# Performance work log

Measured on AMD Instinct MI355X. Metric: run time of the kernel, lower is better.

Reference implementation:

```python
import jax, jax.numpy as jnp
import numpy as np

B, N, INC, H, W = 1, 6, 256, 56, 100
DD, CC = 41, 64                         # depth bins (4..45 step 1), cam feat channels
NX, NY, NZ = 33, 33, 2                  # BEV grid from pc_range=[-50,-50,-5,50,50,3], grid=3
CZ = CC * NZ                            # 128 channels into bevencode
DXV = jnp.array([3.0, 3.0, 3.0], jnp.float32)
BXV = jnp.array([-48.5, -48.5, -3.5], jnp.float32)


def _frustum():
    ds = jnp.arange(4.0, 45.0, 1.0)                      # (41,)
    xs = jnp.linspace(0.0, 1599.0, W)
    ys = jnp.linspace(0.0, 899.0, H)
    d = jnp.broadcast_to(ds[:, None, None], (DD, H, W))
    xg = jnp.broadcast_to(xs[None, None, :], (DD, H, W))
    yg = jnp.broadcast_to(ys[None, :, None], (DD, H, W))
    return jnp.stack([xg, yg, d], -1)                    # (D,H,W,3)


def _conv(x, w):
    return jax.lax.conv_general_dilated(x, w, (1, 1), 'SAME',
                                        dimension_numbers=('NCHW', 'OIHW', 'NCHW'))


def _bn_relu(x, s, b, m, v):
    inv = s / jnp.sqrt(v + 1e-5)
    return jax.nn.relu(x * inv[None, :, None, None] + (b - m * inv)[None, :, None, None])


def _forward(x, rots, trans, dn_w, dn_b,
             bw1, bn1_s, bn1_b, bn1_m, bn1_v,
             bw2, bn2_s, bn2_b, bn2_m, bn2_v,
             bw3, bn3_s, bn3_b, bn3_m, bn3_v,
             bw4, bn4_s, bn4_b, bn4_m, bn4_v):
    # ---- CamEncode: 1x1 depthnet -> softmax depth dist + context features ----
    xf = x.reshape(B * N, INC, H, W)
    y = _conv(xf, dn_w) + dn_b[None, :, None, None]
    depth = jax.nn.softmax(y[:, :DD], axis=1).reshape(B, N, DD, H, W)
    feat = y[:, DD:DD + CC].reshape(B, N, CC, H, W)
    # ---- get_geometry: (u*d, v*d, d) -> ego frame ----
    fr = _frustum()                                                     # (D,H,W,3)
    pts = jnp.concatenate([fr[..., :2] * fr[..., 2:3], fr[..., 2:3]], -1)
    geom = jnp.einsum('bnij,dhwj->bndhwi', rots, pts) + trans[:, :, None, None, None, :]
    # ---- voxel indices (torch .long() truncates toward zero) ----
    coor = ((geom - (BXV - DXV / 2.0)) / DXV).astype(jnp.int32)         # (B,N,D,H,W,3)
    cx, cy, cz = coor[..., 0], coor[..., 1], coor[..., 2]
    kept = (cx >= 0) & (cx < NX) & (cy >= 0) & (cy < NY) & (cz >= 0) & (cz < NZ)
    bidx = jnp.arange(B, dtype=jnp.int32)[:, None, None, None, None]
    ranks = ((bidx * NZ + cz) * NY + cy) * NX + cx                      # bev rank per point
    nvox = B * NZ * NY * NX
    seg = jnp.where(kept, ranks, nvox).reshape(-1)                      # drop bucket = nvox
    # ---- lift: depth-weighted outer product, splat: segment-sum by voxel ----
    vol = depth[..., None] * feat.transpose(0, 1, 3, 4, 2)[:, :, None]  # (B,N,D,H,W,C)
    bev = jax.ops.segment_sum(vol.reshape(-1, CC), seg, num_segments=nvox + 1)[:nvox]
    bev = bev.reshape(B, NZ, NY, NX, CC).transpose(0, 4, 1, 2, 3).reshape(B, CZ, NY, NX)
    h = _bn_relu(_conv(bev, bw1), bn1_s, bn1_b, bn1_m, bn1_v)
    h = _bn_relu(_conv(h, bw2), bn2_s, bn2_b, bn2_m, bn2_v)
    h = _bn_relu(_conv(h, bw3), bn3_s, bn3_b, bn3_m, bn3_v)
    h = _bn_relu(_conv(h, bw4), bn4_s, bn4_b, bn4_m, bn4_v)
    return h                                                            # (B,256,33,33)


def setup_inputs() -> dict:
    key = jax.random.key(0)
    ks = jax.random.split(key, 16)
    x = jax.random.normal(ks[0], (B, N, INC, H, W), jnp.float32)
    # rots = small rotation perturbation composed with intrinsics inverse
    kinv = jnp.array([[1.0 / 800.0, 0.0, -1.0], [0.0, 1.0 / 800.0, -0.5625], [0.0, 0.0, 1.0]], jnp.float32)
    R = jnp.eye(3, dtype=jnp.float32) + 0.05 * jax.random.normal(ks[1], (B, N, 3, 3), jnp.float32)
    rots = jnp.einsum('bnij,jk->bnik', R, kinv)
    trans = 2.0 * jax.random.normal(ks[2], (B, N, 3), jnp.float32)

    def w(k, o, i, kh, kw):
        return jax.random.normal(k, (o, i, kh, kw), jnp.float32) * (2.0 / (i * kh * kw)) ** 0.5

    def bn(k, c):
        k1, k2, k3, k4 = jax.random.split(k, 4)
        return (1.0 + 0.1 * jax.random.normal(k1, (c,), jnp.float32),
                0.1 * jax.random.normal(k2, (c,), jnp.float32),
                0.1 * jax.random.normal(k3, (c,), jnp.float32),
                jax.random.uniform(k4, (c,), jnp.float32, 0.5, 1.5))
    bn1 = bn(ks[7], CZ); bn2 = bn(ks[8], 512); bn3 = bn(ks[9], 512); bn4 = bn(ks[10], 256)
    return dict(
        x=x, rots=rots, trans=trans,
        dn_w=w(ks[3], DD + CC, INC, 1, 1), dn_b=jnp.zeros((DD + CC,), jnp.float32),
        bw1=w(ks[4], CZ, CZ, 3, 3),
        bn1_s=bn1[0], bn1_b=bn1[1], bn1_m=bn1[2], bn1_v=bn1[3],
        bw2=w(ks[5], 512, CZ, 3, 3),
        bn2_s=bn2[0], bn2_b=bn2[1], bn2_m=bn2[2], bn2_v=bn2[3],
        bw3=w(ks[6], 512, 512, 3, 3),
        bn3_s=bn3[0], bn3_b=bn3[1], bn3_m=bn3[2], bn3_v=bn3[3],
        bw4=w(ks[11], 256, 512, 3, 3),
        bn4_s=bn4[0], bn4_b=bn4[1], bn4_m=bn4[2], bn4_v=bn4[3])


def reference(x, rots, trans, dn_w, dn_b,
              bw1, bn1_s, bn1_b, bn1_m, bn1_v,
              bw2, bn2_s, bn2_b, bn2_m, bn2_v,
              bw3, bn3_s, bn3_b, bn3_m, bn3_v,
              bw4, bn4_s, bn4_b, bn4_m, bn4_v):
    return _forward(x, rots, trans, dn_w, dn_b,
                    bw1, bn1_s, bn1_b, bn1_m, bn1_v,
                    bw2, bn2_s, bn2_b, bn2_m, bn2_v,
                    bw3, bn3_s, bn3_b, bn3_m, bn3_v,
                    bw4, bn4_s, bn4_b, bn4_m, bn4_v)
```

## Files before the change

kernel.cpp:

```cpp
#include <hip/hip_runtime.h>
#include <math.h>

#define NCAM  6
#define INC   256
#define HH    56
#define WW    100
#define HW    5600
#define NPIX  33600
#define DDEP  41
#define CFEAT 64
#define NCH   105
#define NXG   33
#define NYG   33
#define NZG   2
#define NVOX  2178
#define PADW  35
#define PADHW 1225
#define NPIXO 1089

typedef short bf16x8 __attribute__((ext_vector_type(8)));
typedef float f32x4  __attribute__((ext_vector_type(4)));

#define Y_OFF    0
#define Y_SZ     (NCAM * NCH * HW)
#define WDH_OFF  (Y_OFF + Y_SZ)
#define WDL_OFF  (WDH_OFF + 16384)
#define W1H_OFF  (WDL_OFF + 16384)
#define W1L_OFF  (W1H_OFF + 73728)
#define W2H_OFF  (W1L_OFF + 73728)
#define W2L_OFF  (W2H_OFF + 294912)
#define W3H_OFF  (W2L_OFF + 294912)
#define W3L_OFF  (W3H_OFF + 1179648)
#define W4H_OFF  (W3L_OFF + 1179648)
#define W4L_OFF  (W4H_OFF + 589824)
#define BEV_OFF  (W4L_OFF + 589824)
#define BEV_SZ   (NVOX * CFEAT)
#define A0_OFF   (BEV_OFF + BEV_SZ)
#define A1_OFF   (A0_OFF + 78400)
#define A2_OFF   (A1_OFF + 78400)
#define A3_OFF   (A2_OFF + 313600)
#define P_OFF    (A3_OFF + 313600)
#define P_SZ     4460544
#define WS_END   (P_OFF + P_SZ)

__device__ __forceinline__ unsigned short f2bf_rn(float f) {
    unsigned u = __builtin_bit_cast(unsigned, f);
    unsigned r = (u + 0x7FFFu + ((u >> 16) & 1u)) >> 16;
    return (unsigned short)r;
}
__device__ __forceinline__ void split_bf(float f, unsigned short& h, unsigned short& l) {
    h = f2bf_rn(f);
    float hf = __builtin_bit_cast(float, (unsigned)h << 16);
    l = f2bf_rn(f - hf);
}
__device__ __forceinline__ void split_bf_trunc(float f, short& h, short& l) {
    unsigned u = __builtin_bit_cast(unsigned, f);
    h = (short)(u >> 16);
    float hf = __builtin_bit_cast(float, u & 0xFFFF0000u);
    float r = f - hf;
    l = (short)(__builtin_bit_cast(unsigned, r) >> 16);
}

__device__ __forceinline__ void wprep_conv(const float* __restrict__ wgt,
                                           unsigned short* __restrict__ wh,
                                           unsigned short* __restrict__ wl,
                                           int COUT, int CIN, int i)
{
    int jj = i & 7, lane = (i >> 3) & 63;
    int r  = i >> 9;
    int nchk = CIN >> 5;
    int chk = r % nchk; r /= nchk;
    int ncog = COUT >> 4;
    int cog = r % ncog; int dydx = r / ncog;
    int co = cog * 16 + (lane & 15);
    int ci = chk * 32 + (lane >> 4) * 8 + jj;
    float w = wgt[((size_t)co * CIN + ci) * 9 + dydx];
    unsigned short h, l; split_bf(w, h, l);
    wh[i] = h; wl[i] = l;
}

__global__ __launch_bounds__(256) void k_wprep_all(const float* __restrict__ dnw,
                                                   const float* __restrict__ bw1,
                                                   const float* __restrict__ bw2,
                                                   const float* __restrict__ bw3,
                                                   const float* __restrict__ bw4,
                                                   unsigned short* __restrict__ wdh,
                                                   unsigned short* __restrict__ wdl,
                                                   unsigned short* __restrict__ w1h,
                                                   unsigned short* __restrict__ w1l,
                                                   unsigned short* __restrict__ w2h,
                                                   unsigned short* __restrict__ w2l,
                                                   unsigned short* __restrict__ w3h,
                                                   unsigned short* __restrict__ w3l,
                                                   unsigned short* __restrict__ w4h,
                                                   unsigned short* __restrict__ w4l)
{
    int i = blockIdx.x * 256 + threadIdx.x;
    if (i < 32768) {
        int jj = i & 7, lane = (i >> 3) & 63, chk = (i >> 9) & 7, ct = i >> 12;
        int co = ct * 16 + (lane & 15);
        int ci = chk * 32 + (lane >> 4) * 8 + jj;
        float w = (co < NCH) ? dnw[co * 256 + ci] : 0.f;
        unsigned short h, l; split_bf(w, h, l);
        wdh[i] = h; wdl[i] = l;
        return;
    }
    i -= 32768;
    if (i < 147456)  { wprep_conv(bw1, w1h, w1l, 128, 128, i); return; }
    i -= 147456;
    if (i < 589824)  { wprep_conv(bw2, w2h, w2l, 512, 128, i); return; }
    i -= 589824;
    if (i < 2359296) { wprep_conv(bw3, w3h, w3l, 512, 512, i); return; }
    i -= 2359296;
    if (i < 1179648) { wprep_conv(bw4, w4h, w4l, 256, 512, i); return; }
}

__global__ __launch_bounds__(256) void k_depthnet_fused(const float* __restrict__ x,
                                                        const unsigned short* __restrict__ wdh,
                                                        const unsigned short* __restrict__ wdl,
                                                        const float* __restrict__ dnb,
                                                        float* __restrict__ y)
{
    const int t  = threadIdx.x;
    const int w  = t >> 6;
    const int l  = t & 63;
    const int lp = l & 15;
    const int q  = l >> 4;
    const int n   = blockIdx.y;
    const int ct0 = blockIdx.z * 4;
    const int px  = blockIdx.x * 64 + w * 16 + lp;
    const bool pok = px < HW;
    const float* xl = x + (size_t)n * INC * HW + (pok ? px : 0);

    f32x4 acc[4];
#pragma unroll
    for (int ct = 0; ct < 4; ++ct) acc[ct] = (f32x4){0.f, 0.f, 0.f, 0.f};

#pragma unroll 2
    for (int ci0 = 0; ci0 < INC; ci0 += 32) {
        float bv[8];
#pragma unroll
        for (int jj = 0; jj < 8; ++jj)
            bv[jj] = xl[(size_t)(ci0 + q * 8 + jj) * HW];
        bf16x8 Bh, Bl;
#pragma unroll
        for (int jj = 0; jj < 8; ++jj) {
            short h, lo; split_bf_trunc(pok ? bv[jj] : 0.f, h, lo);
            Bh[jj] = h; Bl[jj] = lo;
        }
#pragma unroll
        for (int ct = 0; ct < 4; ++ct) {
            const size_t ab = (size_t)(((ct0 + ct) * 8 + (ci0 >> 5)) * 64 + l) * 8;
            bf16x8 Ah = *(const bf16x8*)&wdh[ab];
            bf16x8 Al = *(const bf16x8*)&wdl[ab];
            acc[ct] = __builtin_amdgcn_mfma_f32_16x16x32_bf16(Ah, Bh, acc[ct], 0, 0, 0);
            acc[ct] = __builtin_amdgcn_mfma_f32_16x16x32_bf16(Ah, Bl, acc[ct], 0, 0, 0);
            acc[ct] = __builtin_amdgcn_mfma_f32_16x16x32_bf16(Al, Bh, acc[ct], 0, 0, 0);
        }
    }

    float v[4][4];
#pragma unroll
    for (int ct = 0; ct < 4; ++ct)
#pragma unroll
        for (int j = 0; j < 4; ++j) {
            int co = (ct0 + ct) * 16 + q * 4 + j;
            v[ct][j] = acc[ct][j] + ((co < NCH) ? dnb[co] : 0.f);
        }

    if (ct0 == 0) {
        float m = -3.4e38f;
#pragma unroll
        for (int ct = 0; ct < 4; ++ct)
#pragma unroll
            for (int j = 0; j < 4; ++j) {
                int co = ct * 16 + q * 4 + j;
                if (co < DDEP) m = fmaxf(m, v[ct][j]);
            }
        m = fmaxf(m, __shfl_xor(m, 16));
        m = fmaxf(m, __shfl_xor(m, 32));
        float e[4][4];
        float s = 0.f;
#pragma unroll
        for (int ct = 0; ct < 4; ++ct)
#pragma unroll
            for (int j = 0; j < 4; ++j) {
                int co = ct * 16 + q * 4 + j;
                e[ct][j] = (co < DDEP) ? expf(v[ct][j] - m) : 0.f;
                s += e[ct][j];
            }
        s += __shfl_xor(s, 16);
        s += __shfl_xor(s, 32);
#pragma unroll
        for (int ct = 0; ct < 4; ++ct)
#pragma unroll
            for (int j = 0; j < 4; ++j) {
                int co = ct * 16 + q * 4 + j;
                if (co < DDEP) v[ct][j] = e[ct][j] / s;
            }
    }

    if (pok) {
#pragma unroll
        for (int ct = 0; ct < 4; ++ct)
#pragma unroll
            for (int j = 0; j < 4; ++j) {
                int co = (ct0 + ct) * 16 + q * 4 + j;
                if (co < NCH)
                    y[((size_t)n * NCH + co) * HW + px] = v[ct][j];
            }
    }
}

__global__ __launch_bounds__(256) void k_splat2(const float* __restrict__ y,
                                                const float* __restrict__ rots,
                                                const float* __restrict__ trans,
                                                float* __restrict__ bev)
{
    __shared__ int vox[32 * DDEP];
    const int t  = threadIdx.x;
    const int p0 = blockIdx.x * 32;

    for (int k = t; k < 32 * DDEP; k += 256) {
        int pl = k / DDEP, d = k - pl * DDEP;
        int p = p0 + pl;
        int vx = -1;
        {
            int n = p / HW, hw = p - n * HW;
            int wi = hw % WW, hi = hw / WW;
            const float su = 1599.0f / 99.0f;
            const float sv = 899.0f / 55.0f;
            float u = __fmul_rn((float)wi, su);
            float v = __fmul_rn((float)hi, sv);
            const float* r = rots + n * 9;
            const float* tr = trans + n * 3;
            float dd  = 4.0f + (float)d;
            float pxv = __fmul_rn(u, dd);
            float pyv = __fmul_rn(v, dd);
            float gx = __fadd_rn(__fadd_rn(__fadd_rn(__fmul_rn(r[0], pxv), __fmul_rn(r[1], pyv)), __fmul_rn(r[2], dd)), tr[0]);
            float gy = __fadd_rn(__fadd_rn(__fadd_rn(__fmul_rn(r[3], pxv), __fmul_rn(r[4], pyv)), __fmul_rn(r[5], dd)), tr[1]);
            float gz = __fadd_rn(__fadd_rn(__fadd_rn(__fmul_rn(r[6], pxv), __fmul_rn(r[7], pyv)), __fmul_rn(r[8], dd)), tr[2]);
            int cx = (int)__fdiv_rn(__fadd_rn(gx, 50.0f), 3.0f);
            int cy = (int)__fdiv_rn(__fadd_rn(gy, 50.0f), 3.0f);
            int cz = (int)__fdiv_rn(__fadd_rn(gz, 5.0f), 3.0f);
            if (cx >= 0 && cx < NXG && cy >= 0 && cy < NYG && cz >= 0 && cz < NZG)
                vx = (cz * NYG + cy) * NXG + cx;
        }
        vox[k] = vx;
    }
    __syncthreads();

    const int g  = t >> 5;
    const int pl = t & 31;
    const int p  = p0 + pl;
    int n = p / HW, hw = p - n * HW;
    const float* dbase = y + (size_t)n * NCH * HW + hw;
    const float* fbase = dbase + (size_t)DDEP * HW;
    float f[8];
#pragma unroll
    for (int j = 0; j < 8; ++j) f[j] = fbase[(size_t)(g * 8 + j) * HW];

    float a[8];
#pragma unroll
    for (int j = 0; j < 8; ++j) a[j] = 0.f;
    int cur = -1;
    for (int d = 0; d < DDEP; ++d) {
        int vx = vox[pl * DDEP + d];
        if (vx != cur) {
            if (cur >= 0) {
                float* vp = bev + (size_t)cur * CFEAT + g * 8;
#pragma unroll
                for (int j = 0; j < 8; ++j) atomicAdd(vp + j, a[j]);
            }
            cur = vx;
#pragma unroll
            for (int j = 0; j < 8; ++j) a[j] = 0.f;
        }
        if (vx >= 0) {
            float dval = dbase[(size_t)d * HW];
#pragma unroll
            for (int j = 0; j < 8; ++j) a[j] += __fmul_rn(dval, f[j]);
        }
    }
    if (cur >= 0) {
        float* vp = bev + (size_t)cur * CFEAT + g * 8;
#pragma unroll
        for (int j = 0; j < 8; ++j) atomicAdd(vp + j, a[j]);
    }
}

__global__ __launch_bounds__(256) void k_bev2act(const float* __restrict__ bev,
                                                 unsigned short* __restrict__ a0)
{
    int i = blockIdx.x * 256 + threadIdx.x;
    if (i >= NVOX * CFEAT) return;
    int vx = i >> 6, c = i & 63;
    int cz = vx / NPIXO, rem = vx - cz * NPIXO;
    int yy = rem / NXG, xx = rem - yy * NXG;
    int ch = c * 2 + cz;
    int pos = (yy + 1) * PADW + xx + 1;
    a0[pos * 128 + ch] = f2bf_rn(bev[i]);
}

template<int CIN, int COUT, int SL>
__global__ __launch_bounds__(256) void k_conv_mfma(const unsigned short* __restrict__ act,
                                                   const unsigned short* __restrict__ wh,
                                                   const unsigned short* __restrict__ wl,
                                                   float* __restrict__ P)
{
    constexpr int CI_PER = CIN / SL;
    constexpr int CHUNKS = CI_PER / 32;
    constexpr int NSLOT  = CHUNKS * 4;
    constexpr int SMASK  = NSLOT - 1;
    constexpr int ROW    = NSLOT * 8;
    constexpr int NCOB = COUT / 64;
    constexpr int G    = NCOB * SL;
    constexpr int GX   = G / 8;
    constexpr int POSN = 140;
    __shared__ unsigned short bs[POSN * ROW];
    const int t  = threadIdx.x;
    const int w  = t >> 6;
    const int l  = t & 63;
    const int lp = l & 15;
    const int q  = l >> 4;

    const int bid   = blockIdx.x;
    const int xcd   = bid & 7;
    const int slot  = bid >> 3;
    const int ytile = slot % 17;
    const int gon   = slot / 17;
    const int group = xcd * GX + gon;
    const int cobi  = group % NCOB;
    const int sl    = group / NCOB;

    const int y0  = ytile * 2;
    const int cob = cobi * 64 + w * 16;
    const int ci_base = sl * CI_PER;

    int  pos0[5];
    bool vld[5];
#pragma unroll
    for (int ct = 0; ct < 5; ++ct) {
        int tp = ct * 16 + lp;
        int r = tp / 33, c = tp - r * 33;
        bool v = (tp < 66) && (y0 + r < 33);
        vld[ct]  = v;
        pos0[ct] = v ? (r * 35 + c) : 0;
    }

    for (int i = t; i < POSN * NSLOT; i += 256) {
        int pos = i / NSLOT, s = i - pos * NSLOT;
        int gpos = y0 * 35 + pos;
        int sp = s ^ (pos & SMASK);
        uint4 val = make_uint4(0u, 0u, 0u, 0u);
        if (gpos < PADHW)
            val = *(const uint4*)&act[(size_t)gpos * CIN + ci_base + s * 8];
        *(uint4*)&bs[pos * ROW + sp * 8] = val;
    }
    __syncthreads();

    f32x4 acc[5];
#pragma unroll
    for (int ct = 0; ct < 5; ++ct) acc[ct] = (f32x4){0.f, 0.f, 0.f, 0.f};

#pragma unroll 3
    for (int dydx = 0; dydx < 9; ++dydx) {
        int dy = dydx / 3, dx = dydx - dy * 3;
        int off = dy * 35 + dx;
        bf16x8 Ah[CHUNKS], Al[CHUNKS];
#pragma unroll
        for (int c = 0; c < CHUNKS; ++c) {
            const size_t abase = (size_t)(((dydx * (COUT >> 4) + (cob >> 4)) * (CIN >> 5)
                                           + (ci_base >> 5) + c) * 64 + l) * 8;
            Ah[c] = *(const bf16x8*)&wh[abase];
            Al[c] = *(const bf16x8*)&wl[abase];
        }
#pragma unroll
        for (int ct = 0; ct < 5; ++ct) {
            int pos = pos0[ct] + off;
#pragma unroll
            for (int c = 0; c < CHUNKS; ++c) {
                int sph = (c * 4 + q) ^ (pos & SMASK);
                bf16x8 B = *(const bf16x8*)&bs[pos * ROW + sph * 8];
                acc[ct] = __builtin_amdgcn_mfma_f32_16x16x32_bf16(Ah[c], B, acc[ct], 0, 0, 0);
                acc[ct] = __builtin_amdgcn_mfma_f32_16x16x32_bf16(Al[c], B, acc[ct], 0, 0, 0);
            }
        }
    }

#pragma unroll
    for (int ct = 0; ct < 5; ++ct) {
        if (!vld[ct]) continue;
        int gp = y0 * 33 + ct * 16 + lp;
        float* dst = P + ((size_t)sl * NPIXO + gp) * COUT + cob + q * 4;
        *(f32x4*)dst = acc[ct];
    }
}

template<int SL>
__global__ __launch_bounds__(256) void k_finish(const float* __restrict__ P,
                                                const float* __restrict__ bns,
                                                const float* __restrict__ bnb,
                                                const float* __restrict__ bnm,
                                                const float* __restrict__ bnv,
                                                unsigned short* __restrict__ oact,
                                                float* __restrict__ outf,
                                                int COUT)
{
    int i = blockIdx.x * 256 + threadIdx.x;
    if (i >= COUT * NPIXO) return;
    int co = i % COUT, p = i / COUT;
    float s = 0.f;
#pragma unroll
    for (int sl = 0; sl < SL; ++sl)
        s += P[((size_t)sl * NPIXO + p) * COUT + co];
    float sc = bns[co] / sqrtf(bnv[co] + 1e-5f);
    float bi = bnb[co] - bnm[co] * sc;
    float rv = fmaxf(fmaf(s, sc, bi), 0.f);
    if (outf) {
        outf[(size_t)co * NPIXO + p] = rv;
    } else {
        int yy = p / NXG, xx = p - yy * NXG;
        int pos = (yy + 1) * PADW + xx + 1;
        oact[(size_t)pos * COUT + co] = f2bf_rn(rv);
    }
}

extern "C" void kernel_launch(void* const* d_in, const int* in_sizes, int n_in,
                              void* d_out, int out_size, void* d_ws, size_t ws_size,
                              hipStream_t stream)
{
    const float* x     = (const float*)d_in[0];
    const float* rots  = (const float*)d_in[1];
    const float* trans = (const float*)d_in[2];
    const float* dnw   = (const float*)d_in[3];
    const float* dnb   = (const float*)d_in[4];
    const float* bw1   = (const float*)d_in[5];
    const float* bn1s  = (const float*)d_in[6];
    const float* bn1b  = (const float*)d_in[7];
    const float* bn1m  = (const float*)d_in[8];
    const float* bn1v  = (const float*)d_in[9];
    const float* bw2   = (const float*)d_in[10];
    const float* bn2s  = (const float*)d_in[11];
    const float* bn2b  = (const float*)d_in[12];
    const float* bn2m  = (const float*)d_in[13];
    const float* bn2v  = (const float*)d_in[14];
    const float* bw3   = (const float*)d_in[15];
    const float* bn3s  = (const float*)d_in[16];
    const float* bn3b  = (const float*)d_in[17];
    const float* bn3m  = (const float*)d_in[18];
    const float* bn3v  = (const float*)d_in[19];
    const float* bw4   = (const float*)d_in[20];
    const float* bn4s  = (const float*)d_in[21];
    const float* bn4b  = (const float*)d_in[22];
    const float* bn4m  = (const float*)d_in[23];
    const float* bn4v  = (const float*)d_in[24];

    float* ws  = (float*)d_ws;
    float* y   = ws + Y_OFF;
    float* bev = ws + BEV_OFF;
    float* P   = ws + P_OFF;
    unsigned short* wdh = (unsigned short*)(ws + WDH_OFF);
    unsigned short* wdl = (unsigned short*)(ws + WDL_OFF);
    unsigned short* w1h = (unsigned short*)(ws + W1H_OFF);
    unsigned short* w1l = (unsigned short*)(ws + W1L_OFF);
    unsigned short* w2h = (unsigned short*)(ws + W2H_OFF);
    unsigned short* w2l = (unsigned short*)(ws + W2L_OFF);
    unsigned short* w3h = (unsigned short*)(ws + W3H_OFF);
    unsigned short* w3l = (unsigned short*)(ws + W3L_OFF);
    unsigned short* w4h = (unsigned short*)(ws + W4H_OFF);
    unsigned short* w4l = (unsigned short*)(ws + W4L_OFF);
    unsigned short* a0  = (unsigned short*)(ws + A0_OFF);
    unsigned short* a1  = (unsigned short*)(ws + A1_OFF);
    unsigned short* a2  = (unsigned short*)(ws + A2_OFF);
    unsigned short* a3  = (unsigned short*)(ws + A3_OFF);
    float* out = (float*)d_out;

    hipMemsetAsync(bev, 0, (size_t)(P_OFF - BEV_OFF) * sizeof(float), stream);

    k_wprep_all<<<16832, 256, 0, stream>>>(dnw, bw1, bw2, bw3, bw4,
                                           wdh, wdl, w1h, w1l, w2h, w2l,
                                           w3h, w3l, w4h, w4l);
    k_depthnet_fused<<<dim3(88, 6, 2), 256, 0, stream>>>(x, wdh, wdl, dnb, y);
    k_splat2<<<1050, 256, 0, stream>>>(y, rots, trans, bev);

    k_bev2act<<<(NVOX * CFEAT + 255) / 256, 256, 0, stream>>>(bev, a0);

    k_conv_mfma<128, 128, 4><<<136, 256, 0, stream>>>(a0, w1h, w1l, P);
    k_finish<4><<<(128 * NPIXO + 255) / 256, 256, 0, stream>>>(P, bn1s, bn1b, bn1m, bn1v, a1, nullptr, 128);
    k_conv_mfma<128, 512, 4><<<544, 256, 0, stream>>>(a1, w2h, w2l, P);
    k_finish<4><<<(512 * NPIXO + 255) / 256, 256, 0, stream>>>(P, bn2s, bn2b, bn2m, bn2v, a2, nullptr, 512);
    k_conv_mfma<512, 512, 8><<<1088, 256, 0, stream>>>(a2, w3h, w3l, P);
    k_finish<8><<<(512 * NPIXO + 255) / 256, 256, 0, stream>>>(P, bn3s, bn3b, bn3m, bn3v, a3, nullptr, 512);
    k_conv_mfma<512, 256, 8><<<544, 256, 0, stream>>>(a3, w4h, w4l, P);
    k_finish<8><<<(256 * NPIXO + 255) / 256, 256, 0, stream>>>(P, bn4s, bn4b, bn4m, bn4v, nullptr, out, 256);
}
```

Measured before the change: 118.3 us.

## Fuse BEV zeroing into prep, read BEV directly in conv1, drop memset

```diff
diff --git a/kernel.cpp b/kernel.cpp
--- a/kernel.cpp
+++ b/kernel.cpp
@@ -35,13 +35,14 @@
 #define W4L_OFF  (W4H_OFF + 589824)
 #define BEV_OFF  (W4L_OFF + 589824)
 #define BEV_SZ   (NVOX * CFEAT)
-#define A0_OFF   (BEV_OFF + BEV_SZ)
-#define A1_OFF   (A0_OFF + 78400)
-#define A2_OFF   (A1_OFF + 78400)
+#define A1_OFF   (BEV_OFF + BEV_SZ)
+#define A2_OFF   (A1_OFF + 313600)
 #define A3_OFF   (A2_OFF + 313600)
 #define P_OFF    (A3_OFF + 313600)
 #define P_SZ     4460544
 #define WS_END   (P_OFF + P_SZ)
+
+#define BEV_N4   (BEV_SZ / 4)
 
 __device__ __forceinline__ unsigned short f2bf_rn(float f) {
     unsigned u = __builtin_bit_cast(unsigned, f);
@@ -61,17 +62,18 @@
     l = (short)(__builtin_bit_cast(unsigned, r) >> 16);
 }
 
-__device__ __forceinline__ void wprep_conv(const float* __restrict__ wgt,
-                                           unsigned short* __restrict__ wh,
-                                           unsigned short* __restrict__ wl,
-                                           int COUT, int CIN, int i)
-{
+template<int COUT, int CIN>
+__device__ __forceinline__ void wprep_conv_t(const float* __restrict__ wgt,
+                                             unsigned short* __restrict__ wh,
+                                             unsigned short* __restrict__ wl,
+                                             int i)
+{
+    constexpr int NCHK = CIN >> 5;
+    constexpr int NCOG = COUT >> 4;
     int jj = i & 7, lane = (i >> 3) & 63;
     int r  = i >> 9;
-    int nchk = CIN >> 5;
-    int chk = r % nchk; r /= nchk;
-    int ncog = COUT >> 4;
-    int cog = r % ncog; int dydx = r / ncog;
+    int chk = r % NCHK; r /= NCHK;
+    int cog = r % NCOG; int dydx = r / NCOG;
     int co = cog * 16 + (lane & 15);
     int ci = chk * 32 + (lane >> 4) * 8 + jj;
     float w = wgt[((size_t)co * CIN + ci) * 9 + dydx];
@@ -79,23 +81,26 @@
     wh[i] = h; wl[i] = l;
 }
 
-__global__ __launch_bounds__(256) void k_wprep_all(const float* __restrict__ dnw,
-                                                   const float* __restrict__ bw1,
-                                                   const float* __restrict__ bw2,
-                                                   const float* __restrict__ bw3,
-                                                   const float* __restrict__ bw4,
-                                                   unsigned short* __restrict__ wdh,
-                                                   unsigned short* __restrict__ wdl,
-                                                   unsigned short* __restrict__ w1h,
-                                                   unsigned short* __restrict__ w1l,
-                                                   unsigned short* __restrict__ w2h,
-                                                   unsigned short* __restrict__ w2l,
-                                                   unsigned short* __restrict__ w3h,
-                                                   unsigned short* __restrict__ w3l,
-                                                   unsigned short* __restrict__ w4h,
-                                                   unsigned short* __restrict__ w4l)
+__global__ __launch_bounds__(256) void k_prep(const float* __restrict__ dnw,
+                                              const float* __restrict__ bw1,
+                                              const float* __restrict__ bw2,
+                                              const float* __restrict__ bw3,
+                                              const float* __restrict__ bw4,
+                                              unsigned short* __restrict__ wdh,
+                                              unsigned short* __restrict__ wdl,
+                                              unsigned short* __restrict__ w1h,
+                                              unsigned short* __restrict__ w1l,
+                                              unsigned short* __restrict__ w2h,
+                                              unsigned short* __restrict__ w2l,
+                                              unsigned short* __restrict__ w3h,
+                                              unsigned short* __restrict__ w3l,
+                                              unsigned short* __restrict__ w4h,
+                                              unsigned short* __restrict__ w4l,
+                                              uint4* __restrict__ bev4)
 {
     int i = blockIdx.x * 256 + threadIdx.x;
+    if (i < BEV_N4) { bev4[i] = make_uint4(0u, 0u, 0u, 0u); return; }
+    i -= BEV_N4;
     if (i < 32768) {
         int jj = i & 7, lane = (i >> 3) & 63, chk = (i >> 9) & 7, ct = i >> 12;
         int co = ct * 16 + (lane & 15);
@@ -106,14 +111,15 @@
         return;
     }
     i -= 32768;
-    if (i < 147456)  { wprep_conv(bw1, w1h, w1l, 128, 128, i); return; }
+    if (i < 147456)  { wprep_conv_t<128, 128>(bw1, w1h, w1l, i); return; }
     i -= 147456;
-    if (i < 589824)  { wprep_conv(bw2, w2h, w2l, 512, 128, i); return; }
+    if (i < 589824)  { wprep_conv_t<512, 128>(bw2, w2h, w2l, i); return; }
     i -= 589824;
-    if (i < 2359296) { wprep_conv(bw3, w3h, w3l, 512, 512, i); return; }
+    if (i < 2359296) { wprep_conv_t<512, 512>(bw3, w3h, w3l, i); return; }
     i -= 2359296;
-    if (i < 1179648) { wprep_conv(bw4, w4h, w4l, 256, 512, i); return; }
-}
+    if (i < 1179648) { wprep_conv_t<256, 512>(bw4, w4h, w4l, i); return; }
+}
+#define PREP_TOTAL (BEV_N4 + 32768 + 147456 + 589824 + 2359296 + 1179648)
 
 __global__ __launch_bounds__(256) void k_depthnet_fused(const float* __restrict__ x,
                                                         const unsigned short* __restrict__ wdh,
@@ -289,21 +295,8 @@
     }
 }
 
-__global__ __launch_bounds__(256) void k_bev2act(const float* __restrict__ bev,
-                                                 unsigned short* __restrict__ a0)
-{
-    int i = blockIdx.x * 256 + threadIdx.x;
-    if (i >= NVOX * CFEAT) return;
-    int vx = i >> 6, c = i & 63;
-    int cz = vx / NPIXO, rem = vx - cz * NPIXO;
-    int yy = rem / NXG, xx = rem - yy * NXG;
-    int ch = c * 2 + cz;
-    int pos = (yy + 1) * PADW + xx + 1;
-    a0[pos * 128 + ch] = f2bf_rn(bev[i]);
-}
-
-template<int CIN, int COUT, int SL>
-__global__ __launch_bounds__(256) void k_conv_mfma(const unsigned short* __restrict__ act,
+template<int CIN, int COUT, int SL, int BEVIN>
+__global__ __launch_bounds__(256) void k_conv_mfma(const void* __restrict__ actv,
                                                    const unsigned short* __restrict__ wh,
                                                    const unsigned short* __restrict__ wl,
                                                    float* __restrict__ P)
@@ -318,6 +311,8 @@
     constexpr int GX   = G / 8;
     constexpr int POSN = 140;
     __shared__ unsigned short bs[POSN * ROW];
+    const unsigned short* act = (const unsigned short*)actv;
+    const float* bevf = (const float*)actv;
     const int t  = threadIdx.x;
     const int w  = t >> 6;
     const int l  = t & 63;
@@ -353,8 +348,24 @@
         int gpos = y0 * 35 + pos;
         int sp = s ^ (pos & SMASK);
         uint4 val = make_uint4(0u, 0u, 0u, 0u);
-        if (gpos < PADHW)
-            val = *(const uint4*)&act[(size_t)gpos * CIN + ci_base + s * 8];
+        if (gpos < PADHW) {
+            if constexpr (BEVIN) {
+                int gy = gpos / 35, gx = gpos - gy * 35;
+                if (gy >= 1 && gy <= 33 && gx >= 1 && gx <= 33) {
+                    int vx = (gy - 1) * 33 + (gx - 1);
+                    int c0 = (ci_base + s * 8) >> 1;
+                    float4 v0 = *(const float4*)&bevf[(size_t)vx * 64 + c0];
+                    float4 v1 = *(const float4*)&bevf[(size_t)(NPIXO + vx) * 64 + c0];
+                    unsigned short o[8] = { f2bf_rn(v0.x), f2bf_rn(v1.x),
+                                            f2bf_rn(v0.y), f2bf_rn(v1.y),
+                                            f2bf_rn(v0.z), f2bf_rn(v1.z),
+                                            f2bf_rn(v0.w), f2bf_rn(v1.w) };
+                    val = *(const uint4*)o;
+                }
+            } else {
+                val = *(const uint4*)&act[(size_t)gpos * CIN + ci_base + s * 8];
+            }
+        }
         *(uint4*)&bs[pos * ROW + sp * 8] = val;
     }
     __syncthreads();
@@ -397,32 +408,42 @@
     }
 }
 
-template<int SL>
+template<int SL, int COUT, int FINAL>
 __global__ __launch_bounds__(256) void k_finish(const float* __restrict__ P,
                                                 const float* __restrict__ bns,
                                                 const float* __restrict__ bnb,
                                                 const float* __restrict__ bnm,
                                                 const float* __restrict__ bnv,
                                                 unsigned short* __restrict__ oact,
-                                                float* __restrict__ outf,
-                                                int COUT)
+                                                float* __restrict__ outf)
 {
     int i = blockIdx.x * 256 + threadIdx.x;
-    if (i >= COUT * NPIXO) return;
-    int co = i % COUT, p = i / COUT;
-    float s = 0.f;
-#pragma unroll
-    for (int sl = 0; sl < SL; ++sl)
-        s += P[((size_t)sl * NPIXO + p) * COUT + co];
-    float sc = bns[co] / sqrtf(bnv[co] + 1e-5f);
-    float bi = bnb[co] - bnm[co] * sc;
-    float rv = fmaxf(fmaf(s, sc, bi), 0.f);
-    if (outf) {
-        outf[(size_t)co * NPIXO + p] = rv;
+    constexpr int NP = FINAL ? NPIXO : PADHW;
+    if (i >= COUT * NP) return;
+    int co = i % COUT, pos = i / COUT;
+    if constexpr (FINAL) {
+        float s = 0.f;
+#pragma unroll
+        for (int sl = 0; sl < SL; ++sl)
+            s += P[((size_t)sl * NPIXO + pos) * COUT + co];
+        float sc = bns[co] / sqrtf(bnv[co] + 1e-5f);
+        float bi = bnb[co] - bnm[co] * sc;
+        outf[(size_t)co * NPIXO + pos] = fmaxf(fmaf(s, sc, bi), 0.f);
     } else {
-        int yy = p / NXG, xx = p - yy * NXG;
-        int pos = (yy + 1) * PADW + xx + 1;
-        oact[(size_t)pos * COUT + co] = f2bf_rn(rv);
+        int py = pos / 35, px2 = pos - py * 35;
+        bool inz = (py >= 1) && (py <= 33) && (px2 >= 1) && (px2 <= 33);
+        unsigned short ov = 0;
+        if (inz) {
+            int p = (py - 1) * 33 + (px2 - 1);
+            float s = 0.f;
+#pragma unroll
+            for (int sl = 0; sl < SL; ++sl)
+                s += P[((size_t)sl * NPIXO + p) * COUT + co];
+            float sc = bns[co] / sqrtf(bnv[co] + 1e-5f);
+            float bi = bnb[co] - bnm[co] * sc;
+            ov = f2bf_rn(fmaxf(fmaf(s, sc, bi), 0.f));
+        }
+        oact[(size_t)pos * COUT + co] = ov;
     }
 }
 
@@ -470,28 +491,23 @@
     unsigned short* w3l = (unsigned short*)(ws + W3L_OFF);
     unsigned short* w4h = (unsigned short*)(ws + W4H_OFF);
     unsigned short* w4l = (unsigned short*)(ws + W4L_OFF);
-    unsigned short* a0  = (unsigned short*)(ws + A0_OFF);
     unsigned short* a1  = (unsigned short*)(ws + A1_OFF);
     unsigned short* a2  = (unsigned short*)(ws + A2_OFF);
     unsigned short* a3  = (unsigned short*)(ws + A3_OFF);
     float* out = (float*)d_out;
 
-    hipMemsetAsync(bev, 0, (size_t)(P_OFF - BEV_OFF) * sizeof(float), stream);
-
-    k_wprep_all<<<16832, 256, 0, stream>>>(dnw, bw1, bw2, bw3, bw4,
-                                           wdh, wdl, w1h, w1l, w2h, w2l,
-                                           w3h, w3l, w4h, w4l);
+    k_prep<<<(PREP_TOTAL + 255) / 256, 256, 0, stream>>>(dnw, bw1, bw2, bw3, bw4,
+                                                         wdh, wdl, w1h, w1l, w2h, w2l,
+                                                         w3h, w3l, w4h, w4l, (uint4*)bev);
     k_depthnet_fused<<<dim3(88, 6, 2), 256, 0, stream>>>(x, wdh, wdl, dnb, y);
     k_splat2<<<1050, 256, 0, stream>>>(y, rots, trans, bev);
 
-    k_bev2act<<<(NVOX * CFEAT + 255) / 256, 256, 0, stream>>>(bev, a0);
-
-    k_conv_mfma<128, 128, 4><<<136, 256, 0, stream>>>(a0, w1h, w1l, P);
-    k_finish<4><<<(128 * NPIXO + 255) / 256, 256, 0, stream>>>(P, bn1s, bn1b, bn1m, bn1v, a1, nullptr, 128);
-    k_conv_mfma<128, 512, 4><<<544, 256, 0, stream>>>(a1, w2h, w2l, P);
-    k_finish<4><<<(512 * NPIXO + 255) / 256, 256, 0, stream>>>(P, bn2s, bn2b, bn2m, bn2v, a2, nullptr, 512);
-    k_conv_mfma<512, 512, 8><<<1088, 256, 0, stream>>>(a2, w3h, w3l, P);
-    k_finish<8><<<(512 * NPIXO + 255) / 256, 256, 0, stream>>>(P, bn3s, bn3b, bn3m, bn3v, a3, nullptr, 512);
-    k_conv_mfma<512, 256, 8><<<544, 256, 0, stream>>>(a3, w4h, w4l, P);
-    k_finish<8><<<(256 * NPIXO + 255) / 256, 256, 0, stream>>>(P, bn4s, bn4b, bn4m, bn4v, nullptr, out, 256);
-}
+    k_conv_mfma<128, 128, 4, 1><<<136, 256, 0, stream>>>(bev, w1h, w1l, P);
+    k_finish<4, 128, 0><<<(128 * PADHW + 255) / 256, 256, 0, stream>>>(P, bn1s, bn1b, bn1m, bn1v, a1, nullptr);
+    k_conv_mfma<128, 512, 4, 0><<<544, 256, 0, stream>>>(a1, w2h, w2l, P);
+    k_finish<4, 512, 0><<<(512 * PADHW + 255) / 256, 256, 0, stream>>>(P, bn2s, bn2b, bn2m, bn2v, a2, nullptr);
+    k_conv_mfma<512, 512, 4, 0><<<544, 256, 0, stream>>>(a2, w3h, w3l, P);
+    k_finish<4, 512, 0><<<(512 * PADHW + 255) / 256, 256, 0, stream>>>(P, bn3s, bn3b, bn3m, bn3v, a3, nullptr);
+    k_conv_mfma<512, 256, 8, 0><<<544, 256, 0, stream>>>(a3, w4h, w4l, P);
+    k_finish<8, 256, 1><<<(256 * NPIXO + 255) / 256, 256, 0, stream>>>(P, bn4s, bn4b, bn4m, bn4v, nullptr, out);
+}
```

After: 120.5 us. No clear change (+1.8%).

## Fuse depthnet GEMM with splat via shared-memory tile, drop y buffer

Applied to the files above, without the earlier changes.

```diff
diff --git a/kernel.cpp b/kernel.cpp
--- a/kernel.cpp
+++ b/kernel.cpp
@@ -115,26 +115,32 @@
     if (i < 1179648) { wprep_conv(bw4, w4h, w4l, 256, 512, i); return; }
 }
 
-__global__ __launch_bounds__(256) void k_depthnet_fused(const float* __restrict__ x,
-                                                        const unsigned short* __restrict__ wdh,
-                                                        const unsigned short* __restrict__ wdl,
-                                                        const float* __restrict__ dnb,
-                                                        float* __restrict__ y)
-{
+#define YSTR 66
+__global__ __launch_bounds__(256) void k_dn_splat(const float* __restrict__ x,
+                                                  const unsigned short* __restrict__ wdh,
+                                                  const unsigned short* __restrict__ wdl,
+                                                  const float* __restrict__ dnb,
+                                                  const float* __restrict__ rots,
+                                                  const float* __restrict__ trans,
+                                                  float* __restrict__ bev)
+{
+    __shared__ float ytile[NCH * YSTR];
+    __shared__ int   vox[64 * DDEP];
     const int t  = threadIdx.x;
     const int w  = t >> 6;
     const int l  = t & 63;
     const int lp = l & 15;
     const int q  = l >> 4;
     const int n   = blockIdx.y;
-    const int ct0 = blockIdx.z * 4;
-    const int px  = blockIdx.x * 64 + w * 16 + lp;
+    const int bx  = blockIdx.x;
+    const int pxl = w * 16 + lp;
+    const int px  = bx * 64 + pxl;
     const bool pok = px < HW;
     const float* xl = x + (size_t)n * INC * HW + (pok ? px : 0);
 
-    f32x4 acc[4];
-#pragma unroll
-    for (int ct = 0; ct < 4; ++ct) acc[ct] = (f32x4){0.f, 0.f, 0.f, 0.f};
+    f32x4 acc[7];
+#pragma unroll
+    for (int ct = 0; ct < 7; ++ct) acc[ct] = (f32x4){0.f, 0.f, 0.f, 0.f};
 
 #pragma unroll 2
     for (int ci0 = 0; ci0 < INC; ci0 += 32) {
@@ -149,8 +155,8 @@
             Bh[jj] = h; Bl[jj] = lo;
         }
 #pragma unroll
-        for (int ct = 0; ct < 4; ++ct) {
-            const size_t ab = (size_t)(((ct0 + ct) * 8 + (ci0 >> 5)) * 64 + l) * 8;
+        for (int ct = 0; ct < 7; ++ct) {
+            const size_t ab = (size_t)((ct * 8 + (ci0 >> 5)) * 64 + l) * 8;
             bf16x8 Ah = *(const bf16x8*)&wdh[ab];
             bf16x8 Al = *(const bf16x8*)&wdl[ab];
             acc[ct] = __builtin_amdgcn_mfma_f32_16x16x32_bf16(Ah, Bh, acc[ct], 0, 0, 0);
@@ -159,16 +165,16 @@
         }
     }
 
-    float v[4][4];
-#pragma unroll
-    for (int ct = 0; ct < 4; ++ct)
+    float v[7][4];
+#pragma unroll
+    for (int ct = 0; ct < 7; ++ct)
 #pragma unroll
         for (int j = 0; j < 4; ++j) {
-            int co = (ct0 + ct) * 16 + q * 4 + j;
+            int co = ct * 16 + q * 4 + j;
             v[ct][j] = acc[ct][j] + ((co < NCH) ? dnb[co] : 0.f);
         }
 
-    if (ct0 == 0) {
+    {
         float m = -3.4e38f;
 #pragma unroll
         for (int ct = 0; ct < 4; ++ct)
@@ -200,43 +206,30 @@
             }
     }
 
-    if (pok) {
-#pragma unroll
-        for (int ct = 0; ct < 4; ++ct)
-#pragma unroll
-            for (int j = 0; j < 4; ++j) {
-                int co = (ct0 + ct) * 16 + q * 4 + j;
-                if (co < NCH)
-                    y[((size_t)n * NCH + co) * HW + px] = v[ct][j];
-            }
-    }
-}
-
-__global__ __launch_bounds__(256) void k_splat2(const float* __restrict__ y,
-                                                const float* __restrict__ rots,
-                                                const float* __restrict__ trans,
-                                                float* __restrict__ bev)
-{
-    __shared__ int vox[32 * DDEP];
-    const int t  = threadIdx.x;
-    const int p0 = blockIdx.x * 32;
-
-    for (int k = t; k < 32 * DDEP; k += 256) {
+#pragma unroll
+    for (int ct = 0; ct < 7; ++ct)
+#pragma unroll
+        for (int j = 0; j < 4; ++j) {
+            int co = ct * 16 + q * 4 + j;
+            if (co < NCH) ytile[co * YSTR + pxl] = v[ct][j];
+        }
+    __syncthreads();
+
+    for (int k = t; k < 64 * DDEP; k += 256) {
         int pl = k / DDEP, d = k - pl * DDEP;
-        int p = p0 + pl;
+        int hw = bx * 64 + pl;
         int vx = -1;
-        {
-            int n = p / HW, hw = p - n * HW;
+        if (hw < HW) {
             int wi = hw % WW, hi = hw / WW;
             const float su = 1599.0f / 99.0f;
             const float sv = 899.0f / 55.0f;
             float u = __fmul_rn((float)wi, su);
-            float v = __fmul_rn((float)hi, sv);
+            float vv = __fmul_rn((float)hi, sv);
             const float* r = rots + n * 9;
             const float* tr = trans + n * 3;
             float dd  = 4.0f + (float)d;
             float pxv = __fmul_rn(u, dd);
-            float pyv = __fmul_rn(v, dd);
+            float pyv = __fmul_rn(vv, dd);
             float gx = __fadd_rn(__fadd_rn(__fadd_rn(__fmul_rn(r[0], pxv), __fmul_rn(r[1], pyv)), __fmul_rn(r[2], dd)), tr[0]);
             float gy = __fadd_rn(__fadd_rn(__fadd_rn(__fmul_rn(r[3], pxv), __fmul_rn(r[4], pyv)), __fmul_rn(r[5], dd)), tr[1]);
             float gz = __fadd_rn(__fadd_rn(__fadd_rn(__fmul_rn(r[6], pxv), __fmul_rn(r[7], pyv)), __fmul_rn(r[8], dd)), tr[2]);
@@ -250,42 +243,43 @@
     }
     __syncthreads();
 
-    const int g  = t >> 5;
-    const int pl = t & 31;
-    const int p  = p0 + pl;
-    int n = p / HW, hw = p - n * HW;
-    const float* dbase = y + (size_t)n * NCH * HW + hw;
-    const float* fbase = dbase + (size_t)DDEP * HW;
-    float f[8];
-#pragma unroll
-    for (int j = 0; j < 8; ++j) f[j] = fbase[(size_t)(g * 8 + j) * HW];
-
-    float a[8];
-#pragma unroll
-    for (int j = 0; j < 8; ++j) a[j] = 0.f;
-    int cur = -1;
-    for (int d = 0; d < DDEP; ++d) {
-        int vx = vox[pl * DDEP + d];
-        if (vx != cur) {
-            if (cur >= 0) {
-                float* vp = bev + (size_t)cur * CFEAT + g * 8;
-#pragma unroll
-                for (int j = 0; j < 8; ++j) atomicAdd(vp + j, a[j]);
-            }
-            cur = vx;
-#pragma unroll
-            for (int j = 0; j < 8; ++j) a[j] = 0.f;
-        }
-        if (vx >= 0) {
-            float dval = dbase[(size_t)d * HW];
-#pragma unroll
-            for (int j = 0; j < 8; ++j) a[j] += __fmul_rn(dval, f[j]);
-        }
-    }
-    if (cur >= 0) {
-        float* vp = bev + (size_t)cur * CFEAT + g * 8;
-#pragma unroll
-        for (int j = 0; j < 8; ++j) atomicAdd(vp + j, a[j]);
+    const int g   = t >> 5;
+    const int pl0 = t & 31;
+#pragma unroll 1
+    for (int half = 0; half < 2; ++half) {
+        int pl = pl0 + half * 32;
+        int hw = bx * 64 + pl;
+        if (hw >= HW) continue;
+        float f[8];
+#pragma unroll
+        for (int j = 0; j < 8; ++j) f[j] = ytile[(DDEP + g * 8 + j) * YSTR + pl];
+        float a[8];
+#pragma unroll
+        for (int j = 0; j < 8; ++j) a[j] = 0.f;
+        int cur = -1;
+        for (int d = 0; d < DDEP; ++d) {
+            int vx = vox[pl * DDEP + d];
+            if (vx != cur) {
+                if (cur >= 0) {
+                    float* vp = bev + (size_t)cur * CFEAT + g * 8;
+#pragma unroll
+                    for (int j = 0; j < 8; ++j) atomicAdd(vp + j, a[j]);
+                }
+                cur = vx;
+#pragma unroll
+                for (int j = 0; j < 8; ++j) a[j] = 0.f;
+            }
+            if (vx >= 0) {
+                float dval = ytile[d * YSTR + pl];
+#pragma unroll
+                for (int j = 0; j < 8; ++j) a[j] += __fmul_rn(dval, f[j]);
+            }
+        }
+        if (cur >= 0) {
+            float* vp = bev + (size_t)cur * CFEAT + g * 8;
+#pragma unroll
+            for (int j = 0; j < 8; ++j) atomicAdd(vp + j, a[j]);
+        }
     }
 }
 
@@ -457,7 +451,6 @@
     const float* bn4v  = (const float*)d_in[24];
 
     float* ws  = (float*)d_ws;
-    float* y   = ws + Y_OFF;
     float* bev = ws + BEV_OFF;
     float* P   = ws + P_OFF;
     unsigned short* wdh = (unsigned short*)(ws + WDH_OFF);
@@ -481,8 +474,7 @@
     k_wprep_all<<<16832, 256, 0, stream>>>(dnw, bw1, bw2, bw3, bw4,
                                            wdh, wdl, w1h, w1l, w2h, w2l,
                                            w3h, w3l, w4h, w4l);
-    k_depthnet_fused<<<dim3(88, 6, 2), 256, 0, stream>>>(x, wdh, wdl, dnb, y);
-    k_splat2<<<1050, 256, 0, stream>>>(y, rots, trans, bev);
+    k_dn_splat<<<dim3(88, 6), 256, 0, stream>>>(x, wdh, wdl, dnb, rots, trans, bev);
 
     k_bev2act<<<(NVOX * CFEAT + 255) / 256, 256, 0, stream>>>(bev, a0);
 
```

Result: slower. 121.4 us (+2.6%).
